# Performance work log

Measured on AMD Instinct MI355X. Metric: run time of the kernel, lower is better.

## Reference

```python
import jax, jax.numpy as jnp
import numpy as np

K = 512
D = 64


def setup_inputs() -> dict:
    key = jax.random.key(0)
    k1, k2 = jax.random.split(key)
    z_e_x = jax.random.normal(k1, (32, D, 64, 64), dtype=jnp.float32)  # [B, D, H, W]
    # codebook initialized uniform(-1/K, 1/K) as in the torch module
    emb = jax.random.uniform(k2, (K, D), dtype=jnp.float32, minval=-1.0 / K, maxval=1.0 / K)
    return {"z_e_x": z_e_x, "emb": emb}


def reference(z_e_x, emb):
    B, Dc, H, W = z_e_x.shape
    # [B, D, H, W] -> [B*H*W, D]
    z = jnp.transpose(z_e_x, (0, 2, 3, 1)).reshape(-1, Dc)
    z_norm = jnp.sum(z * z, axis=1, keepdims=True)          # [N, 1]
    e_norm = jnp.sum(emb * emb, axis=1)[None, :]            # [1, K]
    dists = z_norm + e_norm - 2.0 * (z @ emb.T)             # [N, K]
    dists = dists.reshape(B, H, W, -1)
    latents = jnp.argmin(dists, axis=-1)                    # [B, H, W] int
    return latents
```

## Files before the change

kernel.cpp:

```cpp
#include <hip/hip_runtime.h>

#define KCODES 512
#define DDIM   64
#define NROWS  131072

typedef short bf16x8 __attribute__((ext_vector_type(8)));
typedef float f32x4  __attribute__((ext_vector_type(4)));
typedef int   i32x4  __attribute__((ext_vector_type(4)));

union frag_cast { i32x4 i; bf16x8 h; };

__device__ __forceinline__ unsigned f32_to_bf16_rne(float x) {
    unsigned u = __float_as_uint(x);
    return (u + 0x7fffu + ((u >> 16) & 1u)) >> 16;
}

__global__ __launch_bounds__(512) void k1_enorm(const float* __restrict__ emb,
                                                float* __restrict__ en, float* __restrict__ emaxp) {
    __shared__ float red[512];
    int k = threadIdx.x;
    float s = 0.f;
#pragma unroll
    for (int d = 0; d < DDIM; ++d) { float e = emb[k * DDIM + d]; s = fmaf(e, e, s); }
    en[k] = s;
    red[k] = s;
    __syncthreads();
    for (int st = 256; st > 0; st >>= 1) {
        if (k < st) red[k] = fmaxf(red[k], red[k + st]);
        __syncthreads();
    }
    if (k == 0) emaxp[0] = sqrtf(red[0]) * 1.0001f;
}

__global__ __launch_bounds__(128) void k1_efrag(const float* __restrict__ emb,
                                                i32x4* __restrict__ efA, i32x4* __restrict__ efB) {
    int kt = blockIdx.x, t = threadIdx.x;
    int c = t >> 6, lane = t & 63;
    int krow = kt * 16 + (lane & 15);
    int d0 = c * 32 + ((lane >> 4) * 8);
    const float* src = emb + krow * DDIM + d0;
    unsigned hh[8], hl[8];
#pragma unroll
    for (int j = 0; j < 8; ++j) {
        float x = src[j];
        unsigned h = f32_to_bf16_rne(x);
        float hf = __uint_as_float(h << 16);
        hh[j] = h;
        hl[j] = f32_to_bf16_rne(x - hf);
    }
    i32x4 wh, wl;
#pragma unroll
    for (int i = 0; i < 4; ++i) {
        wh[i] = (int)(hh[2 * i] | (hh[2 * i + 1] << 16));
        wl[i] = (int)(hl[2 * i] | (hl[2 * i + 1] << 16));
    }
    efA[(kt * 2 + c) * 64 + lane] = wh;
    efB[(kt * 2 + c) * 64 + lane] = wl;
}

__global__ __launch_bounds__(256, 3) void k3_fused(
    const float* __restrict__ z,
    const i32x4* __restrict__ efA_, const i32x4* __restrict__ efB_,
    const float* __restrict__ en_g, float* __restrict__ zn_g,
    const float* __restrict__ emaxp, int* __restrict__ out,
    int* __restrict__ list, int* __restrict__ cnt) {

    __shared__ i32x4 frag[2048];
    __shared__ float en_l[KCODES];
    __shared__ float zn_l[128];

    const int t = threadIdx.x, blk = blockIdx.x;
    const int n0 = blk * 128;
    const int b = n0 >> 12, hw0 = n0 & 4095;
    const int w = t >> 6, lane = t & 63;
    const int klane = lane & 15, g = lane >> 4;

    i32x4 c0a = efA_[t], c0b = efA_[256 + t];
    i32x4 c0c = efB_[t], c0d = efB_[256 + t];
    float ena = en_g[t], enb = en_g[t + 256];

    const float* zbase = z + (size_t)b * (DDIM * 4096) + hw0;
    float zv[2][16];
#pragma unroll
    for (int tl = 0; tl < 2; ++tl) {
        int row = w * 32 + tl * 16 + klane;
#pragma unroll
        for (int c = 0; c < 2; ++c)
#pragma unroll
            for (int j = 0; j < 8; ++j)
                zv[tl][c * 8 + j] = zbase[(size_t)(c * 32 + g * 8 + j) * 4096 + row];
    }

    frag[t] = c0a; frag[256 + t] = c0b; frag[512 + t] = c0c; frag[768 + t] = c0d;
    en_l[t] = ena; en_l[t + 256] = enb;

    bf16x8 zh[2][2], zl[2][2];
#pragma unroll
    for (int tl = 0; tl < 2; ++tl) {
        float pz = 0.f;
#pragma unroll
        for (int c = 0; c < 2; ++c) {
            unsigned hh[8], hl[8];
#pragma unroll
            for (int j = 0; j < 8; ++j) {
                float x = zv[tl][c * 8 + j];
                pz = fmaf(x, x, pz);
                unsigned h = f32_to_bf16_rne(x);
                float hf = __uint_as_float(h << 16);
                hh[j] = h;
                hl[j] = f32_to_bf16_rne(x - hf);
            }
            frag_cast uh, ul;
#pragma unroll
            for (int i = 0; i < 4; ++i) {
                uh.i[i] = (int)(hh[2 * i] | (hh[2 * i + 1] << 16));
                ul.i[i] = (int)(hl[2 * i] | (hl[2 * i + 1] << 16));
            }
            zh[tl][c] = uh.h;
            zl[tl][c] = ul.h;
        }
        pz += __shfl_xor(pz, 16);
        pz += __shfl_xor(pz, 32);
        if (g == 0) {
            zn_l[w * 32 + tl * 16 + klane] = pz;
            zn_g[n0 + w * 32 + tl * 16 + klane] = pz;
        }
    }
    __syncthreads();

    f32x4 zn4[2];
    zn4[0] = *(const f32x4*)&zn_l[w * 32 + g * 4];
    zn4[1] = *(const f32x4*)&zn_l[w * 32 + 16 + g * 4];
    const float emax = emaxp[0];

    float m1[2][4], m2[2][4];
    int i1[2][4];
#pragma unroll
    for (int tl = 0; tl < 2; ++tl)
#pragma unroll
        for (int r = 0; r < 4; ++r) { m1[tl][r] = 3.4e38f; m2[tl][r] = 3.4e38f; i1[tl][r] = 0; }

    f32x4 zero = {0.f, 0.f, 0.f, 0.f};
    i32x4 lA0, lA1, lB0, lB1;

    for (int c0 = 0; c0 < 8; ++c0) {
        const int buf = c0 & 1;
        if (c0 < 7) {
            int base = (c0 + 1) * 512;
            lA0 = efA_[base + t];       lA1 = efA_[base + 256 + t];
            lB0 = efB_[base + t];       lB1 = efB_[base + 256 + t];
        }
        if (c0 > 0) __syncthreads();

        const bf16x8* fh = (const bf16x8*)&frag[buf * 1024];
        const bf16x8* fl = (const bf16x8*)&frag[buf * 1024 + 512];
#pragma unroll
        for (int ktl = 0; ktl < 4; ++ktl) {
            bf16x8 e0h = fh[(ktl * 2 + 0) * 64 + lane];
            bf16x8 e1h = fh[(ktl * 2 + 1) * 64 + lane];
            bf16x8 e0l = fl[(ktl * 2 + 0) * 64 + lane];
            bf16x8 e1l = fl[(ktl * 2 + 1) * 64 + lane];
            int k = (c0 * 4 + ktl) * 16 + klane;
            float enk = en_l[k];
#pragma unroll
            for (int tl = 0; tl < 2; ++tl) {
                f32x4 acc = __builtin_amdgcn_mfma_f32_16x16x32_bf16(zh[tl][0], e0h, zero, 0, 0, 0);
                acc = __builtin_amdgcn_mfma_f32_16x16x32_bf16(zh[tl][1], e1h, acc, 0, 0, 0);
                acc = __builtin_amdgcn_mfma_f32_16x16x32_bf16(zh[tl][0], e0l, acc, 0, 0, 0);
                acc = __builtin_amdgcn_mfma_f32_16x16x32_bf16(zh[tl][1], e1l, acc, 0, 0, 0);
                acc = __builtin_amdgcn_mfma_f32_16x16x32_bf16(zl[tl][0], e0h, acc, 0, 0, 0);
                acc = __builtin_amdgcn_mfma_f32_16x16x32_bf16(zl[tl][1], e1h, acc, 0, 0, 0);
#pragma unroll
                for (int r = 0; r < 4; ++r) {
                    float d = fmaf(-2.f, acc[r], zn4[tl][r] + enk);
                    float o1 = m1[tl][r];
                    i1[tl][r] = (d < o1) ? k : i1[tl][r];
                    m2[tl][r] = fminf(m2[tl][r], fmaxf(o1, d));
                    m1[tl][r] = fminf(o1, d);
                }
            }
        }
        if (c0 < 7) {
            int base2 = ((c0 + 1) & 1) * 1024;
            frag[base2 + t]             = lA0;
            frag[base2 + 256 + t]       = lA1;
            frag[base2 + 512 + t]       = lB0;
            frag[base2 + 512 + 256 + t] = lB1;
        }
    }

#pragma unroll
    for (int sh = 1; sh <= 8; sh <<= 1) {
#pragma unroll
        for (int tl = 0; tl < 2; ++tl)
#pragma unroll
            for (int r = 0; r < 4; ++r) {
                float om1 = __shfl_xor(m1[tl][r], sh);
                int oi1 = __shfl_xor(i1[tl][r], sh);
                float om2 = __shfl_xor(m2[tl][r], sh);
                float hi = fmaxf(m1[tl][r], om1);
                m2[tl][r] = fminf(fminf(m2[tl][r], om2), hi);
                i1[tl][r] = (om1 < m1[tl][r]) ? oi1 : i1[tl][r];
                m1[tl][r] = fminf(m1[tl][r], om1);
            }
    }

    if (klane == 0) {
#pragma unroll
        for (int tl = 0; tl < 2; ++tl) {
            int rowbase = n0 + w * 32 + tl * 16 + g * 4;
            i32x4 idx4;
#pragma unroll
            for (int r = 0; r < 4; ++r) idx4[r] = i1[tl][r];
            *(i32x4*)(out + rowbase) = idx4;
#pragma unroll
            for (int r = 0; r < 4; ++r) {
                float zz = zn4[tl][r];
                float W = fmaf(sqrtf(zz) * emax, 1.0e-4f, zz * 1.0e-6f);
                if (m2[tl][r] - m1[tl][r] <= W) {
                    int pos = atomicAdd(cnt, 1);
                    list[pos] = rowbase + r;
                }
            }
        }
    }
}

__global__ __launch_bounds__(256) void k4_refine(
    const float* __restrict__ z, const float* __restrict__ emb,
    const float* __restrict__ en, const float* __restrict__ zn_g,
    const int* __restrict__ list, const int* __restrict__ cnt,
    int* __restrict__ out) {
    __shared__ float zrow[4][64];
    int t = threadIdx.x;
    int w = t >> 6, lane = t & 63;
    int nlist = cnt[0];
    for (int li = blockIdx.x * 4 + w; li < nlist; li += gridDim.x * 4) {
        int row = list[li];
        int b = row >> 12, hw = row & 4095;
        const float* zp = z + (size_t)b * (DDIM * 4096) + hw;
        zrow[w][lane] = zp[(size_t)lane * 4096];
        float zn = zn_g[row];
        float best = 3.4e38f;
        int bi = 0;
#pragma unroll 1
        for (int kk = 0; kk < 8; ++kk) {
            int k = lane * 8 + kk;
            const float* e0 = emb + k * DDIM;
            float acc = 0.f;
#pragma unroll
            for (int d = 0; d < DDIM; ++d) acc = fmaf(e0[d], zrow[w][d], acc);
            float dist = fmaf(-2.f, acc, zn + en[k]);
            if (dist < best) { best = dist; bi = k; }
        }
        unsigned long long key =
            ((unsigned long long)__float_as_uint(best) << 32) | (unsigned)bi;
#pragma unroll
        for (int sh = 32; sh; sh >>= 1) {
            unsigned long long o = __shfl_xor(key, sh);
            key = (o < key) ? o : key;
        }
        if (lane == 0) out[row] = (int)(key & 0xFFFFFFFFull);
    }
}

__global__ void fb_enorm(const float* __restrict__ emb, float* __restrict__ en) {
    int k = blockIdx.x * blockDim.x + threadIdx.x;
    if (k < KCODES) {
        float s = 0.f;
#pragma unroll
        for (int d = 0; d < DDIM; ++d) { float e = emb[k * DDIM + d]; s = fmaf(e, e, s); }
        en[k] = s;
    }
}
__global__ __launch_bounds__(256) void fb_argmin(const float* __restrict__ z,
                                                 const float* __restrict__ emb,
                                                 const float* __restrict__ en,
                                                 int* __restrict__ out, int nrows) {
    int n = blockIdx.x * blockDim.x + threadIdx.x;
    if (n >= nrows) return;
    int b = n >> 12, hw = n & 4095;
    const float* zp = z + (size_t)b * (DDIM * 4096) + hw;
    float zr[DDIM];
#pragma unroll
    for (int d = 0; d < DDIM; ++d) zr[d] = zp[(size_t)d * 4096];
    float zn = 0.f;
#pragma unroll
    for (int d = 0; d < DDIM; ++d) zn = fmaf(zr[d], zr[d], zn);
    float best = 3.4e38f; int bi = 0;
    for (int k0 = 0; k0 < KCODES; k0 += 8) {
        float acc[8];
#pragma unroll
        for (int kk = 0; kk < 8; ++kk) acc[kk] = 0.f;
        const float* e0 = emb + k0 * DDIM;
#pragma unroll
        for (int d = 0; d < DDIM; ++d) {
            float zd = zr[d];
#pragma unroll
            for (int kk = 0; kk < 8; ++kk) acc[kk] = fmaf(e0[kk * DDIM + d], zd, acc[kk]);
        }
#pragma unroll
        for (int kk = 0; kk < 8; ++kk) {
            float dist = fmaf(-2.f, acc[kk], zn + en[k0 + kk]);
            if (dist < best) { best = dist; bi = k0 + kk; }
        }
    }
    out[n] = bi;
}

extern "C" void kernel_launch(void* const* d_in, const int* in_sizes, int n_in,
                              void* d_out, int out_size, void* d_ws, size_t ws_size,
                              hipStream_t stream) {
    const float* z   = (const float*)d_in[0];
    const float* emb = (const float*)d_in[1];
    int* out = (int*)d_out;

    const size_t SZ_EF   = 32 * 2 * 64 * 16;
    const size_t SZ_EN   = KCODES * 4;
    const size_t SZ_ZN   = (size_t)NROWS * 4;
    const size_t SZ_EMAX = 64;
    const size_t SZ_LIST = (size_t)NROWS * 4;
    const size_t SZ_CNT  = 64;
    const size_t NEED = 2 * SZ_EF + SZ_EN + SZ_ZN + SZ_EMAX + SZ_LIST + SZ_CNT;

    if (ws_size < NEED) {
        float* en = (float*)d_ws;
        fb_enorm<<<2, 256, 0, stream>>>(emb, en);
        fb_argmin<<<NROWS / 256, 256, 0, stream>>>(z, emb, en, out, NROWS);
        return;
    }

    char* p = (char*)d_ws;
    i32x4* efA = (i32x4*)p;   p += SZ_EF;
    i32x4* efB = (i32x4*)p;   p += SZ_EF;
    float* en  = (float*)p;   p += SZ_EN;
    float* zn  = (float*)p;   p += SZ_ZN;
    float* emaxp = (float*)p; p += SZ_EMAX;
    int* list = (int*)p;      p += SZ_LIST;
    int* cnt  = (int*)p;

    k1_enorm<<<1, 512, 0, stream>>>(emb, en, emaxp);
    k1_efrag<<<32, 128, 0, stream>>>(emb, efA, efB);
    hipMemsetAsync(cnt, 0, 4, stream);

    k3_fused<<<NROWS / 128, 256, 0, stream>>>(z, efA, efB, en, zn, emaxp, out, list, cnt);
    k4_refine<<<512, 256, 0, stream>>>(z, emb, en, zn, list, cnt, out);
}
```

Before: 84.13 us.

## Stream codebook fragments from global/L2 per wave instead of LDS double buffer

Removes the shared-memory double-buffered codebook staging and the per-chunk block barriers. Each wave now loads its codebook fragments directly from global memory, prefetching one k-tile ahead in registers. Launch bounds rise to four blocks per CU to use the freed LDS and registers. Every wave now issues its own global loads of the full codebook, adding L2 traffic and load latency that the compiler must hide.

```diff
diff --git a/kernel.cpp b/kernel.cpp
--- a/kernel.cpp
+++ b/kernel.cpp
@@ -58,14 +58,13 @@
     efB[(kt * 2 + c) * 64 + lane] = wl;
 }
 
-__global__ __launch_bounds__(256, 3) void k3_fused(
+__global__ __launch_bounds__(256, 4) void k3_fused(
     const float* __restrict__ z,
     const i32x4* __restrict__ efA_, const i32x4* __restrict__ efB_,
     const float* __restrict__ en_g, float* __restrict__ zn_g,
     const float* __restrict__ emaxp, int* __restrict__ out,
     int* __restrict__ list, int* __restrict__ cnt) {
 
-    __shared__ i32x4 frag[2048];
     __shared__ float en_l[KCODES];
     __shared__ float zn_l[128];
 
@@ -75,9 +74,8 @@
     const int w = t >> 6, lane = t & 63;
     const int klane = lane & 15, g = lane >> 4;
 
-    i32x4 c0a = efA_[t], c0b = efA_[256 + t];
-    i32x4 c0c = efB_[t], c0d = efB_[256 + t];
-    float ena = en_g[t], enb = en_g[t + 256];
+    en_l[t] = en_g[t];
+    en_l[t + 256] = en_g[t + 256];
 
     const float* zbase = z + (size_t)b * (DDIM * 4096) + hw0;
     float zv[2][16];
@@ -90,9 +88,6 @@
             for (int j = 0; j < 8; ++j)
                 zv[tl][c * 8 + j] = zbase[(size_t)(c * 32 + g * 8 + j) * 4096 + row];
     }
-
-    frag[t] = c0a; frag[256 + t] = c0b; frag[512 + t] = c0c; frag[768 + t] = c0d;
-    en_l[t] = ena; en_l[t + 256] = enb;
 
     bf16x8 zh[2][2], zl[2][2];
 #pragma unroll
@@ -141,52 +136,37 @@
         for (int r = 0; r < 4; ++r) { m1[tl][r] = 3.4e38f; m2[tl][r] = 3.4e38f; i1[tl][r] = 0; }
 
     f32x4 zero = {0.f, 0.f, 0.f, 0.f};
-    i32x4 lA0, lA1, lB0, lB1;
-
-    for (int c0 = 0; c0 < 8; ++c0) {
-        const int buf = c0 & 1;
-        if (c0 < 7) {
-            int base = (c0 + 1) * 512;
-            lA0 = efA_[base + t];       lA1 = efA_[base + 256 + t];
-            lB0 = efB_[base + t];       lB1 = efB_[base + 256 + t];
-        }
-        if (c0 > 0) __syncthreads();
-
-        const bf16x8* fh = (const bf16x8*)&frag[buf * 1024];
-        const bf16x8* fl = (const bf16x8*)&frag[buf * 1024 + 512];
-#pragma unroll
-        for (int ktl = 0; ktl < 4; ++ktl) {
-            bf16x8 e0h = fh[(ktl * 2 + 0) * 64 + lane];
-            bf16x8 e1h = fh[(ktl * 2 + 1) * 64 + lane];
-            bf16x8 e0l = fl[(ktl * 2 + 0) * 64 + lane];
-            bf16x8 e1l = fl[(ktl * 2 + 1) * 64 + lane];
-            int k = (c0 * 4 + ktl) * 16 + klane;
-            float enk = en_l[k];
-#pragma unroll
-            for (int tl = 0; tl < 2; ++tl) {
-                f32x4 acc = __builtin_amdgcn_mfma_f32_16x16x32_bf16(zh[tl][0], e0h, zero, 0, 0, 0);
-                acc = __builtin_amdgcn_mfma_f32_16x16x32_bf16(zh[tl][1], e1h, acc, 0, 0, 0);
-                acc = __builtin_amdgcn_mfma_f32_16x16x32_bf16(zh[tl][0], e0l, acc, 0, 0, 0);
-                acc = __builtin_amdgcn_mfma_f32_16x16x32_bf16(zh[tl][1], e1l, acc, 0, 0, 0);
-                acc = __builtin_amdgcn_mfma_f32_16x16x32_bf16(zl[tl][0], e0h, acc, 0, 0, 0);
-                acc = __builtin_amdgcn_mfma_f32_16x16x32_bf16(zl[tl][1], e1h, acc, 0, 0, 0);
-#pragma unroll
-                for (int r = 0; r < 4; ++r) {
-                    float d = fmaf(-2.f, acc[r], zn4[tl][r] + enk);
-                    float o1 = m1[tl][r];
-                    i1[tl][r] = (d < o1) ? k : i1[tl][r];
-                    m2[tl][r] = fminf(m2[tl][r], fmaxf(o1, d));
-                    m1[tl][r] = fminf(o1, d);
-                }
-            }
-        }
-        if (c0 < 7) {
-            int base2 = ((c0 + 1) & 1) * 1024;
-            frag[base2 + t]             = lA0;
-            frag[base2 + 256 + t]       = lA1;
-            frag[base2 + 512 + t]       = lB0;
-            frag[base2 + 512 + 256 + t] = lB1;
-        }
+
+    i32x4 eh0 = efA_[lane],       eh1 = efA_[64 + lane];
+    i32x4 el0 = efB_[lane],       el1 = efB_[64 + lane];
+#pragma unroll 2
+    for (int kt = 0; kt < 32; ++kt) {
+        int base = ((kt + 1 < 32) ? kt + 1 : 31) * 128;
+        i32x4 nh0 = efA_[base + lane], nh1 = efA_[base + 64 + lane];
+        i32x4 nl0 = efB_[base + lane], nl1 = efB_[base + 64 + lane];
+
+        frag_cast c0h, c1h, c0l, c1l;
+        c0h.i = eh0; c1h.i = eh1; c0l.i = el0; c1l.i = el1;
+        int k = kt * 16 + klane;
+        float enk = en_l[k];
+#pragma unroll
+        for (int tl = 0; tl < 2; ++tl) {
+            f32x4 acc = __builtin_amdgcn_mfma_f32_16x16x32_bf16(zh[tl][0], c0h.h, zero, 0, 0, 0);
+            acc = __builtin_amdgcn_mfma_f32_16x16x32_bf16(zh[tl][1], c1h.h, acc, 0, 0, 0);
+            acc = __builtin_amdgcn_mfma_f32_16x16x32_bf16(zh[tl][0], c0l.h, acc, 0, 0, 0);
+            acc = __builtin_amdgcn_mfma_f32_16x16x32_bf16(zh[tl][1], c1l.h, acc, 0, 0, 0);
+            acc = __builtin_amdgcn_mfma_f32_16x16x32_bf16(zl[tl][0], c0h.h, acc, 0, 0, 0);
+            acc = __builtin_amdgcn_mfma_f32_16x16x32_bf16(zl[tl][1], c1h.h, acc, 0, 0, 0);
+#pragma unroll
+            for (int r = 0; r < 4; ++r) {
+                float d = fmaf(-2.f, acc[r], zn4[tl][r] + enk);
+                float o1 = m1[tl][r];
+                i1[tl][r] = (d < o1) ? k : i1[tl][r];
+                m2[tl][r] = fminf(m2[tl][r], fmaxf(o1, d));
+                m1[tl][r] = fminf(o1, d);
+            }
+        }
+        eh0 = nh0; eh1 = nh1; el0 = nl0; el1 = nl1;
     }
 
 #pragma unroll
```

Result: slower. 87.49 us (+4.0%).
